# Performance work log

Hardware: AMD Instinct MI355X
Metric: run time of the kernel (lower is better)

## Reference

```python
import jax, jax.numpy as jnp
import numpy as np

IN_C = 128
KEY_C = 128
VAL_C = 128
HEADS = 8
N_CLS = 4

def setup_inputs() -> dict:
    key = jax.random.key(0)
    ks = jax.random.split(key, 10)
    n, c, d, h, w = 2, IN_C, 16, 64, 64
    x = jax.random.normal(ks[0], (n, c, d, h, w), dtype=jnp.float32)
    CLS = jax.random.normal(ks[1], (n, KEY_C, N_CLS), dtype=jnp.float32)
    s = 0.02
    Wk = jax.random.normal(ks[2], (KEY_C, IN_C), dtype=jnp.float32) * s
    bk = jnp.zeros((KEY_C,), dtype=jnp.float32)
    Wq = jax.random.normal(ks[3], (KEY_C, IN_C), dtype=jnp.float32) * s
    bq = jnp.zeros((KEY_C,), dtype=jnp.float32)
    Wv = jax.random.normal(ks[4], (VAL_C, IN_C), dtype=jnp.float32) * s
    bv = jnp.zeros((VAL_C,), dtype=jnp.float32)
    Wr = jax.random.normal(ks[5], (IN_C, VAL_C), dtype=jnp.float32) * s
    br = jnp.zeros((IN_C,), dtype=jnp.float32)
    return {"x": x, "CLS": CLS, "Wk": Wk, "bk": bk, "Wq": Wq, "bq": bq,
            "Wv": Wv, "bv": bv, "Wr": Wr, "br": br}

def reference(x, CLS, Wk, bk, Wq, bq, Wv, bv, Wr, br):
    n, c, d, h, w = x.shape
    L = d * h * w
    xf = x.reshape(n, c, L)
    # 1x1 Conv3d == channel matmul
    keys = jnp.einsum('oc,ncl->nol', Wk, xf) + bk[None, :, None]
    queries = jnp.einsum('oc,ncl->nol', Wq, xf) + bq[None, :, None]
    values = jnp.einsum('oc,ncl->nol', Wv, xf) + bv[None, :, None]
    # prepend CLS tokens along the sequence axis
    keys = jnp.concatenate([CLS, keys], axis=-1)      # (n, kc, L+4)
    queries = jnp.concatenate([CLS, queries], axis=-1)
    values = jnp.concatenate([CLS, values], axis=-1)
    Lt = L + N_CLS
    hk = KEY_C // HEADS
    hv = VAL_C // HEADS
    # contiguous channel slices per head == reshape (n, HEADS, hk, Lt)
    k = jax.nn.softmax(keys.reshape(n, HEADS, hk, Lt), axis=3)    # softmax over sequence
    q = jax.nn.softmax(queries.reshape(n, HEADS, hk, Lt), axis=2) # softmax over head channels
    v = values.reshape(n, HEADS, hv, Lt)
    context = jnp.einsum('nhkl,nhvl->nhkv', k, v)                 # (n, H, hk, hv)
    att = jnp.einsum('nhkv,nhkl->nhvl', context, q)               # (n, H, hv, Lt)
    # original loop reassigns CLS each head; final value comes from last head
    CLS_out = att[:, -1, :, :N_CLS]                               # (n, hv, 4)
    agg = att[:, :, :, N_CLS:].reshape(n, HEADS * hv, L)          # concat over heads
    attention = (jnp.einsum('oc,ncl->nol', Wr, agg) + br[None, :, None]).reshape(n, c, d, h, w)
    context_last = context[:, -1]                                 # last head's context
    return (attention, context_last, CLS_out)
```

## Files before the change

kernel.cpp:

```cpp
#include <hip/hip_runtime.h>

typedef unsigned short u16;
typedef short bf16x8 __attribute__((ext_vector_type(8)));
typedef float floatx4 __attribute__((ext_vector_type(4)));

#define L_TOT 65536
#define OUT_CTX 16777216
#define OUT_CLS (OUT_CTX + 512)

__device__ __forceinline__ u16 f2b(float f) {
  unsigned int u = __float_as_uint(f);
  u += 0x7fffu + ((u >> 16) & 1u);
  return (u16)(u >> 16);
}
__device__ __forceinline__ float blo(unsigned int u) { return __uint_as_float(u << 16); }
__device__ __forceinline__ float bhi(unsigned int u) { return __uint_as_float(u & 0xffff0000u); }

__device__ __forceinline__ float pack_val(const float* W, int eo) {
  int mt = eo >> 11;
  int rem = eo & 2047;
  int ks = rem >> 9;
  int lane = (rem >> 3) & 63;
  int j = rem & 7;
  int row = mt * 16 + (lane & 15);
  int col = ks * 32 + (lane >> 4) * 8 + j;
  return W[row * 128 + col];
}

__global__ __launch_bounds__(256) void kP(
    const float* __restrict__ Wk, const float* __restrict__ Wq,
    const float* __restrict__ Wv, const float* __restrict__ Wr,
    const float* __restrict__ CLS,
    float* __restrict__ S2, float* __restrict__ Cnum2,
    u16* __restrict__ wkv, u16* __restrict__ wqf, u16* __restrict__ wrf) {
  const int t = threadIdx.x;
  if (blockIdx.x < 32) {
    #pragma unroll
    for (int i = 0; i < 8; ++i) {
      int e = blockIdx.x * 2048 + i * 256 + t;
      if (e < 32768) {
        wkv[e] = f2b(pack_val(e < 16384 ? Wk : Wv, e & 16383));
      } else if (e < 49152) {
        int eq = e - 32768;
        wqf[eq] = f2b(pack_val(Wq, eq));
      } else {
        int er = e - 49152;
        wrf[er] = f2b(pack_val(Wr, er));
      }
    }
  } else {
    int n = t >> 7, r = t & 127;
    float s = 0.f;
    #pragma unroll
    for (int j = 0; j < 4; ++j) s += __expf(CLS[(n * 128 + r) * 4 + j]);
    S2[n * 128 + r] = s;
    S2[256 + n * 128 + r] = 0.f;
    for (int i = 0; i < 16; ++i) {
      int o = t * 16 + i;
      int nn = o >> 11;
      int rem = o & 2047;
      int h = rem >> 8;
      int kc = (rem >> 4) & 15;
      int vc = rem & 15;
      float a = 0.f;
      #pragma unroll
      for (int j = 0; j < 4; ++j)
        a += __expf(CLS[(nn * 128 + h * 16 + kc) * 4 + j]) *
             CLS[(nn * 128 + h * 16 + vc) * 4 + j];
      Cnum2[o] = a;
      Cnum2[4096 + o] = 0.f;
    }
  }
}

__global__ __launch_bounds__(256) void kA(
    const float* __restrict__ x, const float* __restrict__ bk,
    const float* __restrict__ bv, float* __restrict__ S2,
    float* __restrict__ Cnum2, const u16* __restrict__ wkv) {
  __shared__ __align__(16) u16 xT[64][136];
  __shared__ __align__(16) u16 ev[256][72];
  const int t = threadIdx.x;
  const int w = t >> 6, lane = t & 63;
  const int quad = lane >> 4, lm = lane & 15;
  const int n = blockIdx.x >> 8;
  const int l0base = (blockIdx.x & 255) << 8;
  const int slot = blockIdx.x & 1;

  const int sc = t >> 4;
  const int sl4 = t & 15;

  float4 pf[8];
  #pragma unroll
  for (int i = 0; i < 8; ++i) {
    int c = i * 16 + sc;
    pf[i] = *(const float4*)(x + (((size_t)(n * 128 + c)) << 16) + l0base + sl4 * 4);
  }

  bf16x8 wf[4][4];
  #pragma unroll
  for (int mt = 0; mt < 4; ++mt) {
    int rb = (mt < 2) ? (2 * w + mt) : (8 + 2 * w + (mt - 2));
    #pragma unroll
    for (int ks = 0; ks < 4; ++ks)
      wf[mt][ks] = *(const bf16x8*)(wkv + (((rb * 4 + ks) * 64 + lane) * 8));
  }
  float bias_[4][4];
  #pragma unroll
  for (int mt = 0; mt < 4; ++mt)
    #pragma unroll
    for (int j = 0; j < 4; ++j) {
      int r = w * 32 + (mt & 1) * 16 + quad * 4 + j;
      bias_[mt][j] = (mt < 2) ? bk[r] : bv[r];
    }

  floatx4 z4 = {0.f, 0.f, 0.f, 0.f};
  floatx4 cacc[2] = {z4, z4};
  float sacc = 0.f;

  for (int tile = 0; tile < 4; ++tile) {
    #pragma unroll
    for (int i = 0; i < 8; ++i) {
      int cc = i * 16 + sc;
      int col = sl4 * 4;
      xT[col + 0][cc] = f2b(pf[i].x);
      xT[col + 1][cc] = f2b(pf[i].y);
      xT[col + 2][cc] = f2b(pf[i].z);
      xT[col + 3][cc] = f2b(pf[i].w);
    }
    __syncthreads();

    floatx4 acc[4][4];
    #pragma unroll
    for (int mt = 0; mt < 4; ++mt)
      #pragma unroll
      for (int nt = 0; nt < 4; ++nt) acc[mt][nt] = z4;

    #pragma unroll
    for (int nt = 0; nt < 4; ++nt)
      #pragma unroll
      for (int ks = 0; ks < 4; ++ks) {
        bf16x8 b = *(const bf16x8*)(&xT[nt * 16 + lm][ks * 32 + quad * 8]);
        #pragma unroll
        for (int mt = 0; mt < 4; ++mt)
          acc[mt][nt] = __builtin_amdgcn_mfma_f32_16x16x32_bf16(wf[mt][ks], b, acc[mt][nt], 0, 0, 0);
      }

    #pragma unroll
    for (int mt = 0; mt < 4; ++mt)
      #pragma unroll
      for (int j = 0; j < 4; ++j) {
        int R = ((mt < 2) ? 0 : 128) + w * 32 + (mt & 1) * 16 + quad * 4 + j;
        #pragma unroll
        for (int nt = 0; nt < 4; ++nt) {
          float v = acc[mt][nt][j] + bias_[mt][j];
          if (mt < 2) v = __expf(v);
          ev[R][nt * 16 + lm] = f2b(v);
        }
      }

    if (tile < 3) {
      int l0 = l0base + (tile + 1) * 64;
      #pragma unroll
      for (int i = 0; i < 8; ++i) {
        int c = i * 16 + sc;
        pf[i] = *(const float4*)(x + (((size_t)(n * 128 + c)) << 16) + l0 + sl4 * 4);
      }
    }
    __syncthreads();

    #pragma unroll
    for (int hh = 0; hh < 2; ++hh) {
      int h = w * 2 + hh;
      #pragma unroll
      for (int ks = 0; ks < 2; ++ks) {
        bf16x8 aE = *(const bf16x8*)(&ev[h * 16 + lm][ks * 32 + quad * 8]);
        bf16x8 bV = *(const bf16x8*)(&ev[128 + h * 16 + lm][ks * 32 + quad * 8]);
        cacc[hh] = __builtin_amdgcn_mfma_f32_16x16x32_bf16(aE, bV, cacc[hh], 0, 0, 0);
      }
    }
    if (t < 128) {
      #pragma unroll
      for (int i = 0; i < 8; ++i) {
        uint4 u = *(const uint4*)(&ev[t][i * 8]);
        sacc += blo(u.x) + bhi(u.x) + blo(u.y) + bhi(u.y) +
                blo(u.z) + bhi(u.z) + blo(u.w) + bhi(u.w);
      }
    }
  }

  float* Cn = Cnum2 + slot * 4096;
  #pragma unroll
  for (int hh = 0; hh < 2; ++hh) {
    int h = w * 2 + hh;
    #pragma unroll
    for (int j = 0; j < 4; ++j)
      atomicAdd(&Cn[((n * 8 + h) * 16 + quad * 4 + j) * 16 + lm], cacc[hh][j]);
  }
  if (t < 128) atomicAdd(&S2[slot * 256 + n * 128 + t], sacc);
}

__global__ __launch_bounds__(256) void kB(
    const float* __restrict__ x, const float* __restrict__ bq,
    const float* __restrict__ br, const u16* __restrict__ wqf,
    const u16* __restrict__ wrf, const float* __restrict__ S2,
    const float* __restrict__ Cnum2, const float* __restrict__ CLS,
    float* __restrict__ out) {
  __shared__ __align__(16) u16 xT[64][136];
  __shared__ __align__(16) u16 qT[64][136];
  __shared__ __align__(16) u16 aT[64][136];
  const int t = threadIdx.x;
  const int w = t >> 6, lane = t & 63;
  const int quad = lane >> 4, lm = lane & 15;
  const int n = blockIdx.x >> 8;
  const int l0base = (blockIdx.x & 255) << 8;

  const int sc = t >> 4;
  const int sl4 = t & 15;

  float4 pf[8];
  #pragma unroll
  for (int i = 0; i < 8; ++i) {
    int c = i * 16 + sc;
    pf[i] = *(const float4*)(x + (((size_t)(n * 128 + c)) << 16) + l0base + sl4 * 4);
  }

  bf16x8 wq[2][4], wr[2][4];
  #pragma unroll
  for (int mt = 0; mt < 2; ++mt)
    #pragma unroll
    for (int ks = 0; ks < 4; ++ks) {
      wq[mt][ks] = *(const bf16x8*)(wqf + ((((w * 2 + mt) * 4 + ks) * 64 + lane) * 8));
      wr[mt][ks] = *(const bf16x8*)(wrf + ((((w * 2 + mt) * 4 + ks) * 64 + lane) * 8));
    }

  bf16x8 aC[2];
  #pragma unroll
  for (int mt = 0; mt < 2; ++mt) {
    int h = w * 2 + mt;
    short frag[8];
    #pragma unroll
    for (int j = 0; j < 8; ++j) {
      int k = quad * 8 + j;
      float v = 0.f;
      if (k < 16) {
        int ci = ((n * 8 + h) * 16 + k) * 16 + lm;
        float c = Cnum2[ci] + Cnum2[4096 + ci];
        float s = S2[n * 128 + h * 16 + k] + S2[256 + n * 128 + h * 16 + k];
        v = c / s;
      }
      frag[j] = (short)f2b(v);
    }
    aC[mt] = *(bf16x8*)frag;
  }

  if (blockIdx.x == 0) {
    for (int e = t; e < 512; e += 256) {
      int nn = e >> 8;
      int kc = (e >> 4) & 15;
      int vc = e & 15;
      int ci = ((nn * 8 + 7) * 16 + kc) * 16 + vc;
      float c = Cnum2[ci] + Cnum2[4096 + ci];
      float s = S2[nn * 128 + 112 + kc] + S2[256 + nn * 128 + 112 + kc];
      out[OUT_CTX + e] = c / s;
    }
    if (t < 128) {
      int nn = t >> 6;
      int vc = (t >> 2) & 15;
      int j = t & 3;
      float den = 0.f, num = 0.f;
      #pragma unroll
      for (int kc = 0; kc < 16; ++kc) {
        float e_ = __expf(CLS[(nn * 128 + 112 + kc) * 4 + j]);
        int ci = ((nn * 8 + 7) * 16 + kc) * 16 + vc;
        float c = Cnum2[ci] + Cnum2[4096 + ci];
        float s = S2[nn * 128 + 112 + kc] + S2[256 + nn * 128 + 112 + kc];
        den += e_;
        num += e_ * (c / s);
      }
      out[OUT_CLS + t] = num / den;
    }
  }

  float bqv_[2][4], brv[2][4];
  #pragma unroll
  for (int mt = 0; mt < 2; ++mt)
    #pragma unroll
    for (int j = 0; j < 4; ++j) {
      bqv_[mt][j] = bq[(w * 2 + mt) * 16 + quad * 4 + j];
      brv[mt][j] = br[(w * 2 + mt) * 16 + quad * 4 + j];
    }

  floatx4 z4 = {0.f, 0.f, 0.f, 0.f};

  for (int tile = 0; tile < 4; ++tile) {
    int l0 = l0base + tile * 64;
    #pragma unroll
    for (int i = 0; i < 8; ++i) {
      int cc = i * 16 + sc;
      int col = sl4 * 4;
      xT[col + 0][cc] = f2b(pf[i].x);
      xT[col + 1][cc] = f2b(pf[i].y);
      xT[col + 2][cc] = f2b(pf[i].z);
      xT[col + 3][cc] = f2b(pf[i].w);
    }
    __syncthreads();

    floatx4 acc[2][4];
    #pragma unroll
    for (int mt = 0; mt < 2; ++mt)
      #pragma unroll
      for (int nt = 0; nt < 4; ++nt) acc[mt][nt] = z4;

    #pragma unroll
    for (int nt = 0; nt < 4; ++nt)
      #pragma unroll
      for (int ks = 0; ks < 4; ++ks) {
        bf16x8 b = *(const bf16x8*)(&xT[nt * 16 + lm][ks * 32 + quad * 8]);
        #pragma unroll
        for (int mt = 0; mt < 2; ++mt)
          acc[mt][nt] = __builtin_amdgcn_mfma_f32_16x16x32_bf16(wq[mt][ks], b, acc[mt][nt], 0, 0, 0);
      }

    #pragma unroll
    for (int mt = 0; mt < 2; ++mt) {
      int h = w * 2 + mt;
      #pragma unroll
      for (int nt = 0; nt < 4; ++nt) {
        float e[4];
        float ssum = 0.f;
        #pragma unroll
        for (int j = 0; j < 4; ++j) {
          e[j] = __expf(acc[mt][nt][j] + bqv_[mt][j]);
          ssum += e[j];
        }
        ssum += __shfl_xor(ssum, 16);
        ssum += __shfl_xor(ssum, 32);
        float inv = 1.f / ssum;
        #pragma unroll
        for (int j = 0; j < 4; ++j)
          qT[nt * 16 + lm][h * 16 + quad * 4 + j] = f2b(e[j] * inv);
      }
    }

    #pragma unroll
    for (int mt = 0; mt < 2; ++mt) {
      int h = w * 2 + mt;
      #pragma unroll
      for (int nt = 0; nt < 4; ++nt) {
        bf16x8 bq_ = *(const bf16x8*)(&qT[nt * 16 + lm][h * 16 + (quad & 1) * 8]);
        floatx4 d = __builtin_amdgcn_mfma_f32_16x16x32_bf16(aC[mt], bq_, z4, 0, 0, 0);
        #pragma unroll
        for (int j = 0; j < 4; ++j)
          aT[nt * 16 + lm][h * 16 + quad * 4 + j] = f2b(d[j]);
      }
    }

    if (tile < 3) {
      int l0n = l0base + (tile + 1) * 64;
      #pragma unroll
      for (int i = 0; i < 8; ++i) {
        int c = i * 16 + sc;
        pf[i] = *(const float4*)(x + (((size_t)(n * 128 + c)) << 16) + l0n + sl4 * 4);
      }
    }
    __syncthreads();

    floatx4 acc2[2][4];
    #pragma unroll
    for (int mt = 0; mt < 2; ++mt)
      #pragma unroll
      for (int nt = 0; nt < 4; ++nt) acc2[mt][nt] = z4;

    #pragma unroll
    for (int nt = 0; nt < 4; ++nt)
      #pragma unroll
      for (int ks = 0; ks < 4; ++ks) {
        bf16x8 b = *(const bf16x8*)(&aT[nt * 16 + lm][ks * 32 + quad * 8]);
        #pragma unroll
        for (int mt = 0; mt < 2; ++mt)
          acc2[mt][nt] = __builtin_amdgcn_mfma_f32_16x16x32_bf16(wr[mt][ks], b, acc2[mt][nt], 0, 0, 0);
      }

    #pragma unroll
    for (int mt = 0; mt < 2; ++mt)
      #pragma unroll
      for (int j = 0; j < 4; ++j) {
        int R = (w * 2 + mt) * 16 + quad * 4 + j;
        #pragma unroll
        for (int nt = 0; nt < 4; ++nt)
          out[(((size_t)(n * 128 + R)) << 16) + l0 + nt * 16 + lm] = acc2[mt][nt][j] + brv[mt][j];
      }
  }
}

extern "C" void kernel_launch(void* const* d_in, const int* in_sizes, int n_in,
                              void* d_out, int out_size, void* d_ws, size_t ws_size,
                              hipStream_t stream) {
  const float* x   = (const float*)d_in[0];
  const float* CLS = (const float*)d_in[1];
  const float* Wk  = (const float*)d_in[2];
  const float* bk  = (const float*)d_in[3];
  const float* Wq  = (const float*)d_in[4];
  const float* bq  = (const float*)d_in[5];
  const float* Wv  = (const float*)d_in[6];
  const float* bv  = (const float*)d_in[7];
  const float* Wr  = (const float*)d_in[8];
  const float* br  = (const float*)d_in[9];
  float* out = (float*)d_out;
  char* ws = (char*)d_ws;
  float* S2    = (float*)(ws + 0);
  float* Cnum2 = (float*)(ws + 2048);
  u16* wkv     = (u16*)(ws + 34816);
  u16* wqf     = (u16*)(ws + 100352);
  u16* wrf     = (u16*)(ws + 133120);

  kP<<<33, 256, 0, stream>>>(Wk, Wq, Wv, Wr, CLS, S2, Cnum2, wkv, wqf, wrf);
  kA<<<512, 256, 0, stream>>>(x, bk, bv, S2, Cnum2, wkv);
  kB<<<512, 256, 0, stream>>>(x, bq, br, wqf, wrf, S2, Cnum2, CLS, out);
}
```

Measured before the change: 167.9 us.

## Fold per-head context into output projection weights via a separate small kernel

Adds a single-block kernel that builds, for each batch, the combined matrix M = Wr · blockdiag(context_h) as packed bf16 MFMA fragments, and writes the last-head context and CLS outputs. kB then runs one 128x128 MFMA GEMM on the softmaxed queries instead of first applying a per-head context MFMA, staging the result in LDS and then applying Wr. This removes one MFMA stage, one LDS buffer and a sync-dependent round trip per tile. In exchange it adds a serial one-block launch between kA and kB and rounds the fused matrix to bf16.

```diff
diff --git a/kernel.cpp b/kernel.cpp
--- a/kernel.cpp
+++ b/kernel.cpp
@@ -29,23 +29,19 @@
 
 __global__ __launch_bounds__(256) void kP(
     const float* __restrict__ Wk, const float* __restrict__ Wq,
-    const float* __restrict__ Wv, const float* __restrict__ Wr,
-    const float* __restrict__ CLS,
+    const float* __restrict__ Wv, const float* __restrict__ CLS,
     float* __restrict__ S2, float* __restrict__ Cnum2,
-    u16* __restrict__ wkv, u16* __restrict__ wqf, u16* __restrict__ wrf) {
+    u16* __restrict__ wkv, u16* __restrict__ wqf) {
   const int t = threadIdx.x;
-  if (blockIdx.x < 32) {
+  if (blockIdx.x < 24) {
     #pragma unroll
     for (int i = 0; i < 8; ++i) {
       int e = blockIdx.x * 2048 + i * 256 + t;
       if (e < 32768) {
         wkv[e] = f2b(pack_val(e < 16384 ? Wk : Wv, e & 16383));
-      } else if (e < 49152) {
+      } else {
         int eq = e - 32768;
         wqf[eq] = f2b(pack_val(Wq, eq));
-      } else {
-        int er = e - 49152;
-        wrf[er] = f2b(pack_val(Wr, er));
       }
     }
   } else {
@@ -199,15 +195,72 @@
   if (t < 128) atomicAdd(&S2[slot * 256 + n * 128 + t], sacc);
 }
 
+__global__ __launch_bounds__(256) void kF(
+    const float* __restrict__ Wr, const float* __restrict__ CLS,
+    const float* __restrict__ S2, const float* __restrict__ Cnum2,
+    u16* __restrict__ Mf, float* __restrict__ out) {
+  __shared__ float WrS[128 * 129];
+  __shared__ float ctxS[4096];
+  const int t = threadIdx.x;
+  for (int i = 0; i < 64; ++i) {
+    int e = i * 256 + t;
+    WrS[(e >> 7) * 129 + (e & 127)] = Wr[e];
+  }
+  for (int i = 0; i < 16; ++i) {
+    int o = i * 256 + t;
+    int n = o >> 11;
+    int rem = o & 2047;
+    int h = rem >> 8;
+    int kc = (rem >> 4) & 15;
+    int vc = o & 15;
+    float c = Cnum2[o] + Cnum2[4096 + o];
+    float s = S2[n * 128 + h * 16 + kc] + S2[256 + n * 128 + h * 16 + kc];
+    float v = c / s;
+    ctxS[o] = v;
+    if (h == 7) out[OUT_CTX + (n * 16 + kc) * 16 + vc] = v;
+  }
+  __syncthreads();
+  if (t < 128) {
+    int n = t >> 6;
+    int vc = (t >> 2) & 15;
+    int j = t & 3;
+    float den = 0.f, num = 0.f;
+    #pragma unroll
+    for (int kc = 0; kc < 16; ++kc) {
+      float e_ = __expf(CLS[(n * 128 + 112 + kc) * 4 + j]);
+      den += e_;
+      num += e_ * ctxS[((n * 8 + 7) * 16 + kc) * 16 + vc];
+    }
+    out[OUT_CLS + t] = num / den;
+  }
+  const int lane = t & 63, g = t >> 6;
+  for (int idx = 0; idx < 16; ++idx) {
+    int combo = g * 16 + idx;
+    int n = combo >> 5;
+    int mtile = (combo >> 2) & 7;
+    int ks = combo & 3;
+    int o = mtile * 16 + (lane & 15);
+    u16 frag[8];
+    #pragma unroll
+    for (int j = 0; j < 8; ++j) {
+      int c = ks * 32 + (lane >> 4) * 8 + j;
+      int h = c >> 4, kc = c & 15;
+      float m = 0.f;
+      #pragma unroll
+      for (int vc = 0; vc < 16; ++vc)
+        m += WrS[o * 129 + h * 16 + vc] * ctxS[((n * 8 + h) * 16 + kc) * 16 + vc];
+      frag[j] = f2b(m);
+    }
+    *(uint4*)(Mf + ((size_t)combo * 64 + lane) * 8) = *(uint4*)frag;
+  }
+}
+
 __global__ __launch_bounds__(256) void kB(
     const float* __restrict__ x, const float* __restrict__ bq,
     const float* __restrict__ br, const u16* __restrict__ wqf,
-    const u16* __restrict__ wrf, const float* __restrict__ S2,
-    const float* __restrict__ Cnum2, const float* __restrict__ CLS,
-    float* __restrict__ out) {
+    const u16* __restrict__ Mf, float* __restrict__ out) {
   __shared__ __align__(16) u16 xT[64][136];
   __shared__ __align__(16) u16 qT[64][136];
-  __shared__ __align__(16) u16 aT[64][136];
   const int t = threadIdx.x;
   const int w = t >> 6, lane = t & 63;
   const int quad = lane >> 4, lm = lane & 15;
@@ -224,62 +277,14 @@
     pf[i] = *(const float4*)(x + (((size_t)(n * 128 + c)) << 16) + l0base + sl4 * 4);
   }
 
-  bf16x8 wq[2][4], wr[2][4];
+  bf16x8 wq[2][4], mf[2][4];
   #pragma unroll
   for (int mt = 0; mt < 2; ++mt)
     #pragma unroll
     for (int ks = 0; ks < 4; ++ks) {
       wq[mt][ks] = *(const bf16x8*)(wqf + ((((w * 2 + mt) * 4 + ks) * 64 + lane) * 8));
-      wr[mt][ks] = *(const bf16x8*)(wrf + ((((w * 2 + mt) * 4 + ks) * 64 + lane) * 8));
-    }
-
-  bf16x8 aC[2];
-  #pragma unroll
-  for (int mt = 0; mt < 2; ++mt) {
-    int h = w * 2 + mt;
-    short frag[8];
-    #pragma unroll
-    for (int j = 0; j < 8; ++j) {
-      int k = quad * 8 + j;
-      float v = 0.f;
-      if (k < 16) {
-        int ci = ((n * 8 + h) * 16 + k) * 16 + lm;
-        float c = Cnum2[ci] + Cnum2[4096 + ci];
-        float s = S2[n * 128 + h * 16 + k] + S2[256 + n * 128 + h * 16 + k];
-        v = c / s;
-      }
-      frag[j] = (short)f2b(v);
-    }
-    aC[mt] = *(bf16x8*)frag;
-  }
-
-  if (blockIdx.x == 0) {
-    for (int e = t; e < 512; e += 256) {
-      int nn = e >> 8;
-      int kc = (e >> 4) & 15;
-      int vc = e & 15;
-      int ci = ((nn * 8 + 7) * 16 + kc) * 16 + vc;
-      float c = Cnum2[ci] + Cnum2[4096 + ci];
-      float s = S2[nn * 128 + 112 + kc] + S2[256 + nn * 128 + 112 + kc];
-      out[OUT_CTX + e] = c / s;
-    }
-    if (t < 128) {
-      int nn = t >> 6;
-      int vc = (t >> 2) & 15;
-      int j = t & 3;
-      float den = 0.f, num = 0.f;
-      #pragma unroll
-      for (int kc = 0; kc < 16; ++kc) {
-        float e_ = __expf(CLS[(nn * 128 + 112 + kc) * 4 + j]);
-        int ci = ((nn * 8 + 7) * 16 + kc) * 16 + vc;
-        float c = Cnum2[ci] + Cnum2[4096 + ci];
-        float s = S2[nn * 128 + 112 + kc] + S2[256 + nn * 128 + 112 + kc];
-        den += e_;
-        num += e_ * (c / s);
-      }
-      out[OUT_CLS + t] = num / den;
-    }
-  }
+      mf[mt][ks] = *(const bf16x8*)(Mf + ((((size_t)(n * 8 + w * 2 + mt) * 4 + ks) * 64 + lane) * 8));
+    }
 
   float bqv_[2][4], brv[2][4];
   #pragma unroll
@@ -342,19 +347,6 @@
       }
     }
 
-    #pragma unroll
-    for (int mt = 0; mt < 2; ++mt) {
-      int h = w * 2 + mt;
-      #pragma unroll
-      for (int nt = 0; nt < 4; ++nt) {
-        bf16x8 bq_ = *(const bf16x8*)(&qT[nt * 16 + lm][h * 16 + (quad & 1) * 8]);
-        floatx4 d = __builtin_amdgcn_mfma_f32_16x16x32_bf16(aC[mt], bq_, z4, 0, 0, 0);
-        #pragma unroll
-        for (int j = 0; j < 4; ++j)
-          aT[nt * 16 + lm][h * 16 + quad * 4 + j] = f2b(d[j]);
-      }
-    }
-
     if (tile < 3) {
       int l0n = l0base + (tile + 1) * 64;
       #pragma unroll
@@ -375,10 +367,10 @@
     for (int nt = 0; nt < 4; ++nt)
       #pragma unroll
       for (int ks = 0; ks < 4; ++ks) {
-        bf16x8 b = *(const bf16x8*)(&aT[nt * 16 + lm][ks * 32 + quad * 8]);
+        bf16x8 b = *(const bf16x8*)(&qT[nt * 16 + lm][ks * 32 + quad * 8]);
         #pragma unroll
         for (int mt = 0; mt < 2; ++mt)
-          acc2[mt][nt] = __builtin_amdgcn_mfma_f32_16x16x32_bf16(wr[mt][ks], b, acc2[mt][nt], 0, 0, 0);
+          acc2[mt][nt] = __builtin_amdgcn_mfma_f32_16x16x32_bf16(mf[mt][ks], b, acc2[mt][nt], 0, 0, 0);
       }
 
     #pragma unroll
@@ -412,9 +404,10 @@
   float* Cnum2 = (float*)(ws + 2048);
   u16* wkv     = (u16*)(ws + 34816);
   u16* wqf     = (u16*)(ws + 100352);
-  u16* wrf     = (u16*)(ws + 133120);
-
-  kP<<<33, 256, 0, stream>>>(Wk, Wq, Wv, Wr, CLS, S2, Cnum2, wkv, wqf, wrf);
+  u16* Mf      = (u16*)(ws + 133120);
+
+  kP<<<25, 256, 0, stream>>>(Wk, Wq, Wv, CLS, S2, Cnum2, wkv, wqf);
   kA<<<512, 256, 0, stream>>>(x, bk, bv, S2, Cnum2, wkv);
-  kB<<<512, 256, 0, stream>>>(x, bq, br, wqf, wrf, S2, Cnum2, CLS, out);
-}
+  kF<<<1, 256, 0, stream>>>(Wr, CLS, S2, Cnum2, Mf, out);
+  kB<<<512, 256, 0, stream>>>(x, bq, br, wqf, Mf, out);
+}
```

After: 183.0 us. +9.0%, slower.
